# Optimization experiments

Hardware: AMD Instinct MI355X
Metric: run time of the kernel (lower is better)

The kernel has to match this reference:

```python
import jax, jax.numpy as jnp
import numpy as np

B, CIN, H, W = 256, 1280, 7, 7
A, NCLS, HID, NGT = 9, 20, 128, 40
OUT_DIM = 5 * A + NCLS  # 65


def setup_inputs() -> dict:
    key = jax.random.key(0)
    ks = jax.random.split(key, 8)
    features = jax.random.normal(ks[0], (B, CIN, H, W), jnp.float32)
    # grid: (x, y) centers of each feature cell, in feature-map coordinates
    grid = jax.random.uniform(ks[1], (B, H, W, 2), jnp.float32) * 7.0
    # GT boxes (x1, y1, x2, y2, class), padded count NGT per image
    xy1 = jax.random.uniform(ks[2], (B, NGT, 2), jnp.float32) * 5.0
    wh = jax.random.uniform(ks[3], (B, NGT, 2), jnp.float32) * 2.0 + 0.5
    cls = jax.random.randint(ks[4], (B, NGT, 1), 0, NCLS).astype(jnp.float32)
    bboxes = jnp.concatenate([xy1, xy1 + wh, cls], axis=-1)
    # anchor shapes (w, h) as in SingleStageDetector.__init__
    anc = jnp.array([[1.0, 1], [2, 2], [3, 3], [4, 4], [5, 5],
                     [2, 3], [3, 2], [3, 5], [5, 3]], jnp.float32)
    W1 = jax.random.normal(ks[5], (HID, CIN), jnp.float32) * 0.02
    b1 = jnp.zeros((HID,), jnp.float32)
    W2 = jax.random.normal(ks[6], (OUT_DIM, HID), jnp.float32) * 0.02
    b2 = jnp.zeros((OUT_DIM,), jnp.float32)
    return dict(features=features, grid=grid, bboxes=bboxes, anc=anc,
                W1=W1, b1=b1, W2=W2, b2=b2)


def reference(features, grid, bboxes, anc, W1, b1, W2, b2):
    Bx = features.shape[0]
    # --- PredictionNetwork (inference mode; dropout is identity at eval) ---
    h = jnp.einsum('bchw,oc->bohw', features, W1) + b1[None, :, None, None]
    h = jax.nn.leaky_relu(h, negative_slope=0.01)
    out = jnp.einsum('bchw,oc->bohw', h, W2) + b2[None, :, None, None]
    conf_scores = jax.nn.sigmoid(out[:, 4 * A:5 * A])          # (B, A, H, W)
    offsets = out[:, :4 * A].reshape(Bx, A, 4, H, W)
    offsets = jnp.concatenate(
        [jax.nn.sigmoid(offsets[:, :, :2]) - 0.5, offsets[:, :, 2:]], axis=2)
    class_scores = out[:, 5 * A:]                               # (B, C, H, W)
    # --- GenerateAnchor: (B, A, H, W, 4) as (x_tl, y_tl, x_br, y_br) ---
    ctr = grid[:, None]                    # (B, 1, H, W, 2)
    half = anc[None, :, None, None, :] / 2  # (1, A, 1, 1, 2)
    anchors = jnp.concatenate([ctr - half, ctr + half], axis=-1)
    # --- IoU: (B, A*H*W, N) ---
    P = anchors.reshape(Bx, -1, 4)          # (B, AHW, 4)
    gt = bboxes[..., :4]                    # (B, N, 4)
    tl = jnp.maximum(P[:, :, None, :2], gt[:, None, :, :2])
    br = jnp.minimum(P[:, :, None, 2:], gt[:, None, :, 2:])
    inter = jnp.prod(jnp.clip(br - tl, 0.0), axis=-1)  # (B, AHW, N)
    # torch code zeroes intersections for proposals with any coord <= 0
    legal = (jnp.min(P, axis=-1) > 0)[..., None]
    inter = inter * legal
    p_area = ((P[:, :, 2] - P[:, :, 0]) * (P[:, :, 3] - P[:, :, 1]))[:, :, None]
    g_area = ((gt[:, :, 2] - gt[:, :, 0]) * (gt[:, :, 3] - gt[:, :, 1]))[:, None, :]
    iou_mat = inter / (g_area + p_area - inter)
    return (conf_scores, offsets, class_scores, iou_mat)
```

## Files before the change

### kernel.cpp

```cpp
#include <hip/hip_runtime.h>


#define CIN_  1280
#define HW_   49
#define HID_  128
#define OUTD_ 65
#define NGT_  40
#define NP_   441
#define NCH   20

#define CONF_OFF 0
#define OFFS_OFF 112896
#define CLS_OFF  564480
#define IOU_OFF  815360

#define W1F_U32  81920

#define SF_STRIDE 644
#define SF_SIZE   (49 * SF_STRIDE)

typedef __bf16 bf16x8 __attribute__((ext_vector_type(8)));
typedef float  f32x4  __attribute__((ext_vector_type(4)));

__device__ __forceinline__ unsigned pack2bf(float lo, float hi) {
    unsigned a = __float_as_uint(lo);
    unsigned b = __float_as_uint(hi);
    a = (a + 0x7FFFu + ((a >> 16) & 1u)) >> 16;
    b = (b + 0x7FFFu + ((b >> 16) & 1u)) >> 16;
    return a | (b << 16);
}
__device__ __forceinline__ float bflo(unsigned u) { return __uint_as_float(u << 16); }
__device__ __forceinline__ float bfhi(unsigned u) { return __uint_as_float(u & 0xFFFF0000u); }
__device__ __forceinline__ float sigmoidf_(float v) { return 1.f / (1.f + __expf(-v)); }

__device__ __forceinline__ bf16x8 ld_frag(const unsigned* p) {
    union { uint4 u; bf16x8 v; } x;
    x.u = *(const uint4*)p;
    return x.v;
}
__device__ __forceinline__ bf16x8 as_bf(uint4 u) {
    union { uint4 u; bf16x8 v; } x; x.u = u; return x.v;
}

__global__ __launch_bounds__(256) void prep_w1(const float* __restrict__ W1,
                                               unsigned* __restrict__ gW1f) {
    int X = blockIdx.x * 256 + threadIdx.x;
    int sub  = X & 3;
    int lane = (X >> 2) & 63;
    int r    = X >> 8;
    int ks   = r & 1;
    int w    = (r >> 1) & 7;
    int ch   = r >> 4;
    int o = w * 16 + (lane & 15);
    int c = ch * 64 + ks * 32 + (lane >> 4) * 8 + sub * 2;
    float2 f = *(const float2*)(W1 + o * CIN_ + c);
    gW1f[X] = pack2bf(f.x, f.y);
}

__global__ __launch_bounds__(512) void fused_kernel(
    const float* __restrict__ F,
    const float* __restrict__ grid,
    const float* __restrict__ bbox,
    const float* __restrict__ anc,
    const unsigned* __restrict__ gW1f,
    const float* __restrict__ B1,
    const float* __restrict__ W2,
    const float* __restrict__ B2,
    float* __restrict__ out)
{
    __shared__ unsigned lds[SF_SIZE];
    unsigned* smF = lds;
    unsigned* smH = lds;
    float* smP = (float*)(lds + 3136);
    float* smG = (float*)(lds + 3136 + 2646);

    const int tid  = threadIdx.x;
    const int b    = blockIdx.x;
    const int lane = tid & 63;
    const int w    = tid >> 6;
    const int quad = lane >> 4;
    const int m16  = lane & 15;

    const float* Fb = F + b * (CIN_ * HW_);

    for (int i = tid; i < 640 * 49; i += 512) {
        int cp = i / 49;
        int hw = i - cp * 49;
        const float* s = Fb + (2 * cp) * HW_ + hw;
        smF[hw * SF_STRIDE + cp] = pack2bf(s[0], s[HW_]);
    }
    __syncthreads();

    const int row3 = (m16 == 0) ? 48 : (m16 - 1);
    const unsigned* Bb[4] = {
        smF + (0 * 16 + m16) * SF_STRIDE + quad * 4,
        smF + (1 * 16 + m16) * SF_STRIDE + quad * 4,
        smF + (2 * 16 + m16) * SF_STRIDE + quad * 4,
        smF + row3 * SF_STRIDE + quad * 4
    };

    const uint4* Aw = (const uint4*)gW1f + (w * 2) * 64 + lane;

    f32x4 acc[4];
    #pragma unroll
    for (int nt = 0; nt < 4; ++nt) acc[nt] = (f32x4)(0.f);

    uint4 a0 = Aw[0];
    uint4 a1 = Aw[64];
    for (int ch = 0; ch < NCH; ++ch) {
        uint4 na0, na1;
        if (ch < NCH - 1) {
            na0 = Aw[(ch + 1) * 1024];
            na1 = Aw[(ch + 1) * 1024 + 64];
        }
        const int coff = ch * 32;
        bf16x8 aa0 = as_bf(a0);
        bf16x8 aa1 = as_bf(a1);
        #pragma unroll
        for (int nt = 0; nt < 4; ++nt) {
            bf16x8 b0 = ld_frag(Bb[nt] + coff);
            bf16x8 b1 = ld_frag(Bb[nt] + coff + 16);
            acc[nt] = __builtin_amdgcn_mfma_f32_16x16x32_bf16(aa0, b0, acc[nt], 0, 0, 0);
            acc[nt] = __builtin_amdgcn_mfma_f32_16x16x32_bf16(aa1, b1, acc[nt], 0, 0, 0);
        }
        a0 = na0; a1 = na1;
    }

    __syncthreads();

    #pragma unroll
    for (int nt = 0; nt < 4; ++nt) {
        int hw = (nt < 3) ? (nt * 16 + m16) : ((m16 == 0) ? 48 : -1);
        if (hw >= 0) {
            #pragma unroll
            for (int rp = 0; rp < 2; ++rp) {
                int o0 = w * 16 + quad * 4 + 2 * rp;
                float v0 = acc[nt][2 * rp]     + B1[o0];
                float v1 = acc[nt][2 * rp + 1] + B1[o0 + 1];
                v0 = v0 > 0.f ? v0 : 0.01f * v0;
                v1 = v1 > 0.f ? v1 : 0.01f * v1;
                smH[(o0 >> 1) * HW_ + hw] = pack2bf(v0, v1);
            }
        }
    }

    if (tid < NP_) {
        int pp = tid, a = pp / 49, r = pp - a * 49;
        float cx = grid[b * 98 + 2 * r], cy = grid[b * 98 + 2 * r + 1];
        float hx = anc[2 * a] * 0.5f,    hy = anc[2 * a + 1] * 0.5f;
        float x1 = cx - hx, y1 = cy - hy, x2 = cx + hx, y2 = cy + hy;
        smP[pp * 6 + 0] = x1; smP[pp * 6 + 1] = y1;
        smP[pp * 6 + 2] = x2; smP[pp * 6 + 3] = y2;
        smP[pp * 6 + 4] = (x2 - x1) * (y2 - y1);
        smP[pp * 6 + 5] = (fminf(fminf(x1, y1), fminf(x2, y2)) > 0.f) ? 1.f : 0.f;
    }
    if (tid >= 472) {
        int g = tid - 472;
        float x1 = bbox[b * 200 + g * 5 + 0];
        float y1 = bbox[b * 200 + g * 5 + 1];
        float x2 = bbox[b * 200 + g * 5 + 2];
        float y2 = bbox[b * 200 + g * 5 + 3];
        smG[g * 5 + 0] = x1; smG[g * 5 + 1] = y1;
        smG[g * 5 + 2] = x2; smG[g * 5 + 3] = y2;
        smG[g * 5 + 4] = (x2 - x1) * (y2 - y1);
    }
    __syncthreads();

    for (int idx = tid; idx < OUTD_ * HW_; idx += 512) {
        int o2 = idx / 49;
        int hw = idx - o2 * 49;
        const float2* wr = (const float2*)(W2 + o2 * HID_);
        float s0 = 0.f, s1 = 0.f;
        #pragma unroll 8
        for (int k2 = 0; k2 < 64; ++k2) {
            unsigned hp = smH[k2 * HW_ + hw];
            float2 wv = wr[k2];
            s0 = fmaf(wv.x, bflo(hp), s0);
            s1 = fmaf(wv.y, bfhi(hp), s1);
        }
        float a = B2[o2] + (s0 + s1);

        unsigned int dst;
        float val;
        if (o2 < 36) {
            int an = o2 >> 2, kk = o2 & 3;
            val = (kk < 2) ? (sigmoidf_(a) - 0.5f) : a;
            dst = OFFS_OFF + b * 1764 + an * 196 + kk * 49 + hw;
        } else if (o2 < 45) {
            val = sigmoidf_(a);
            dst = CONF_OFF + b * 441 + (o2 - 36) * 49 + hw;
        } else {
            val = a;
            dst = CLS_OFF + b * 980 + (o2 - 45) * 49 + hw;
        }
        out[dst] = val;
    }

    for (int idx = tid; idx < NP_ * NGT_; idx += 512) {
        int pp = idx / 40;
        int g  = idx - pp * 40;
        const float* P = smP + pp * 6;
        const float* G = smG + g * 5;
        float tlx = fmaxf(P[0], G[0]);
        float tly = fmaxf(P[1], G[1]);
        float brx = fminf(P[2], G[2]);
        float bry = fminf(P[3], G[3]);
        float dx = fmaxf(brx - tlx, 0.f);
        float dy = fmaxf(bry - tly, 0.f);
        float inter = dx * dy * P[5];
        out[IOU_OFF + b * (NP_ * NGT_) + idx] = inter / (G[4] + P[4] - inter);
    }
}

__global__ __launch_bounds__(512) void fused_fallback(
    const float* __restrict__ F, const float* __restrict__ grid,
    const float* __restrict__ bbox, const float* __restrict__ anc,
    const float* __restrict__ W1, const float* __restrict__ B1,
    const float* __restrict__ W2, const float* __restrict__ B2,
    float* __restrict__ out)
{
    __shared__ unsigned lds[4608 + 2304 + 6272];
    unsigned* smA = lds;
    unsigned* smB = lds + 4608;
    float*    smH = (float*)(lds + 4608 + 2304);
    float* smP = (float*)lds;
    float* smG = (float*)(lds + 4608);

    const int tid  = threadIdx.x;
    const int b    = blockIdx.x;
    const int lane = tid & 63;
    const int w    = tid >> 6;
    const int quad = lane >> 4;
    const int m16  = lane & 15;
    const float* Fb = F + b * (CIN_ * HW_);

    f32x4 acc[4];
    #pragma unroll
    for (int nt = 0; nt < 4; ++nt) acc[nt] = (f32x4)(0.f);

    for (int ch = 0; ch < NCH; ++ch) {
        const int c0 = ch * 64;
        __syncthreads();
        #pragma unroll
        for (int rr = 0; rr < 8; ++rr) {
            int pi = tid + rr * 512;
            int o = pi >> 5, cp = pi & 31;
            float2 fx = *(const float2*)(W1 + o * CIN_ + c0 + 2 * cp);
            smA[o * 36 + cp] = pack2bf(fx.x, fx.y);
        }
        for (int pi = tid; pi < 32 * 49; pi += 512) {
            int cp = pi / 49;
            int hw = pi - cp * 49;
            const float* src = Fb + (c0 + 2 * cp) * HW_ + hw;
            smB[hw * 36 + cp] = pack2bf(src[0], src[HW_]);
        }
        __syncthreads();
        const unsigned* Ab = smA + (w * 16 + m16) * 36 + quad * 4;
        const unsigned* Bb = smB + m16 * 36 + quad * 4;
        #pragma unroll
        for (int ks = 0; ks < 2; ++ks) {
            bf16x8 af = ld_frag(Ab + ks * 16);
            #pragma unroll
            for (int nt = 0; nt < 4; ++nt) {
                bf16x8 bf = ld_frag(Bb + nt * 16 * 36 + ks * 16);
                acc[nt] = __builtin_amdgcn_mfma_f32_16x16x32_bf16(af, bf, acc[nt], 0, 0, 0);
            }
        }
    }
    #pragma unroll
    for (int nt = 0; nt < 4; ++nt) {
        int hw = nt * 16 + m16;
        if (hw < HW_) {
            #pragma unroll
            for (int r = 0; r < 4; ++r) {
                int o = w * 16 + quad * 4 + r;
                float v = acc[nt][r] + B1[o];
                v = v > 0.f ? v : 0.01f * v;
                smH[o * HW_ + hw] = v;
            }
        }
    }
    __syncthreads();
    if (tid < NP_) {
        int pp = tid, a = pp / 49, r = pp - a * 49;
        float cx = grid[b * 98 + 2 * r], cy = grid[b * 98 + 2 * r + 1];
        float hx = anc[2 * a] * 0.5f,    hy = anc[2 * a + 1] * 0.5f;
        float x1 = cx - hx, y1 = cy - hy, x2 = cx + hx, y2 = cy + hy;
        smP[pp * 6 + 0] = x1; smP[pp * 6 + 1] = y1;
        smP[pp * 6 + 2] = x2; smP[pp * 6 + 3] = y2;
        smP[pp * 6 + 4] = (x2 - x1) * (y2 - y1);
        smP[pp * 6 + 5] = (fminf(fminf(x1, y1), fminf(x2, y2)) > 0.f) ? 1.f : 0.f;
    }
    if (tid >= 472) {
        int g = tid - 472;
        float x1 = bbox[b * 200 + g * 5 + 0];
        float y1 = bbox[b * 200 + g * 5 + 1];
        float x2 = bbox[b * 200 + g * 5 + 2];
        float y2 = bbox[b * 200 + g * 5 + 3];
        smG[g * 5 + 0] = x1; smG[g * 5 + 1] = y1;
        smG[g * 5 + 2] = x2; smG[g * 5 + 3] = y2;
        smG[g * 5 + 4] = (x2 - x1) * (y2 - y1);
    }
    for (int idx = tid; idx < OUTD_ * HW_; idx += 512) {
        int o2 = idx / 49;
        int hw = idx - o2 * 49;
        const float4* wr = (const float4*)(W2 + o2 * HID_);
        const float*  hc = smH + hw;
        float s0 = 0.f, s1 = 0.f, s2 = 0.f, s3 = 0.f;
        #pragma unroll 8
        for (int k4 = 0; k4 < 32; ++k4) {
            float4 wv = wr[k4];
            s0 = fmaf(wv.x, hc[(4 * k4 + 0) * HW_], s0);
            s1 = fmaf(wv.y, hc[(4 * k4 + 1) * HW_], s1);
            s2 = fmaf(wv.z, hc[(4 * k4 + 2) * HW_], s2);
            s3 = fmaf(wv.w, hc[(4 * k4 + 3) * HW_], s3);
        }
        float a = B2[o2] + ((s0 + s1) + (s2 + s3));
        unsigned int dst; float val;
        if (o2 < 36) { int an = o2 >> 2, kk = o2 & 3;
            val = (kk < 2) ? (sigmoidf_(a) - 0.5f) : a;
            dst = OFFS_OFF + b * 1764 + an * 196 + kk * 49 + hw;
        } else if (o2 < 45) { val = sigmoidf_(a);
            dst = CONF_OFF + b * 441 + (o2 - 36) * 49 + hw;
        } else { val = a;
            dst = CLS_OFF + b * 980 + (o2 - 45) * 49 + hw; }
        out[dst] = val;
    }
    __syncthreads();
    for (int idx = tid; idx < NP_ * NGT_; idx += 512) {
        int pp = idx / 40;
        int g  = idx - pp * 40;
        const float* P = smP + pp * 6;
        const float* G = smG + g * 5;
        float tlx = fmaxf(P[0], G[0]);
        float tly = fmaxf(P[1], G[1]);
        float brx = fminf(P[2], G[2]);
        float bry = fminf(P[3], G[3]);
        float dx = fmaxf(brx - tlx, 0.f);
        float dy = fmaxf(bry - tly, 0.f);
        float inter = dx * dy * P[5];
        out[IOU_OFF + b * (NP_ * NGT_) + idx] = inter / (G[4] + P[4] - inter);
    }
}

extern "C" void kernel_launch(void* const* d_in, const int* in_sizes, int n_in,
                              void* d_out, int out_size, void* d_ws, size_t ws_size,
                              hipStream_t stream) {
    const float* F  = (const float*)d_in[0];
    const float* G  = (const float*)d_in[1];
    const float* BB = (const float*)d_in[2];
    const float* AN = (const float*)d_in[3];
    const float* W1 = (const float*)d_in[4];
    const float* B1 = (const float*)d_in[5];
    const float* W2 = (const float*)d_in[6];
    const float* B2 = (const float*)d_in[7];
    float* out = (float*)d_out;

    if (ws_size >= (size_t)W1F_U32 * 4) {
        unsigned* gW1f = (unsigned*)d_ws;
        prep_w1<<<320, 256, 0, stream>>>(W1, gW1f);
        fused_kernel<<<256, 512, 0, stream>>>(F, G, BB, AN, gW1f, B1, W2, B2, out);
    } else {
        fused_fallback<<<256, 512, 0, stream>>>(F, G, BB, AN, W1, B1, W2, B2, out);
    }
}
```

Before: 141.3 us.

## Split GEMM1 along K across four blocks per image, add MFMA GEMM2 epilogue kernel

The first GEMM is split along the input-channel dimension into four blocks per image (1024 blocks instead of 256), so more CUs work on the feature load and MFMA loop. Each block writes bf16 partial sums to workspace, and the IoU work is spread across the four blocks. A second kernel reduces the partials, applies bias and leaky-ReLU, and runs the 65x128 head through MFMA with pre-packed bf16 W2. In exchange it adds extra launches, a workspace round-trip for the partials, and more rounding because the partials are stored in bf16.

```diff
diff --git a/kernel.cpp b/kernel.cpp
--- a/kernel.cpp
+++ b/kernel.cpp
@@ -7,17 +7,17 @@
 #define OUTD_ 65
 #define NGT_  40
 #define NP_   441
-#define NCH   20
 
 #define CONF_OFF 0
 #define OFFS_OFF 112896
 #define CLS_OFF  564480
 #define IOU_OFF  815360
 
-#define W1F_U32  81920
-
-#define SF_STRIDE 644
-#define SF_SIZE   (49 * SF_STRIDE)
+#define WS_W1F   0
+#define WS_W2F   81920
+#define WS_PART  87040
+#define WS_NEED_FULL ((87040u + 3211264u) * 4u)
+#define WS_NEED_MID  (81920u * 4u)
 
 typedef __bf16 bf16x8 __attribute__((ext_vector_type(8)));
 typedef float  f32x4  __attribute__((ext_vector_type(4)));
@@ -42,37 +42,161 @@
     union { uint4 u; bf16x8 v; } x; x.u = u; return x.v;
 }
 
-__global__ __launch_bounds__(256) void prep_w1(const float* __restrict__ W1,
-                                               unsigned* __restrict__ gW1f) {
+__global__ __launch_bounds__(256) void prep_w1f(const float* __restrict__ W1,
+                                                unsigned* __restrict__ g) {
     int X = blockIdx.x * 256 + threadIdx.x;
-    int sub  = X & 3;
-    int lane = (X >> 2) & 63;
-    int r    = X >> 8;
-    int ks   = r & 1;
-    int w    = (r >> 1) & 7;
-    int ch   = r >> 4;
-    int o = w * 16 + (lane & 15);
-    int c = ch * 64 + ks * 32 + (lane >> 4) * 8 + sub * 2;
-    float2 f = *(const float2*)(W1 + o * CIN_ + c);
-    gW1f[X] = pack2bf(f.x, f.y);
-}
-
-__global__ __launch_bounds__(512) void fused_kernel(
-    const float* __restrict__ F,
-    const float* __restrict__ grid,
-    const float* __restrict__ bbox,
-    const float* __restrict__ anc,
+    int sub = X & 3, lane = (X >> 2) & 63, f = X >> 8;
+    int mt = f & 7, K32 = f >> 3;
+    int o = mt * 16 + (lane & 15);
+    int c = K32 * 32 + (lane >> 4) * 8 + sub * 2;
+    float2 v = *(const float2*)(W1 + o * CIN_ + c);
+    g[X] = pack2bf(v.x, v.y);
+}
+
+__global__ __launch_bounds__(256) void prep_w2f(const float* __restrict__ W2,
+                                                unsigned* __restrict__ g) {
+    int X = blockIdx.x * 256 + threadIdx.x;
+    int sub = X & 3, lane = (X >> 2) & 63, f = X >> 8;
+    int mt2 = f % 5, ks2 = f / 5;
+    int o2 = mt2 * 16 + (lane & 15);
+    int c = ks2 * 32 + (lane >> 4) * 8 + sub * 2;
+    unsigned val = 0;
+    if (o2 < OUTD_) {
+        float2 v = *(const float2*)(W2 + o2 * HID_ + c);
+        val = pack2bf(v.x, v.y);
+    }
+    g[X] = val;
+}
+
+__global__ __launch_bounds__(256) void gemm1_partial(
+    const float* __restrict__ F, const float* __restrict__ grid,
+    const float* __restrict__ bbox, const float* __restrict__ anc,
     const unsigned* __restrict__ gW1f,
-    const float* __restrict__ B1,
-    const float* __restrict__ W2,
-    const float* __restrict__ B2,
+    unsigned* __restrict__ wsp, float* __restrict__ out)
+{
+    __shared__ __align__(16) unsigned smF[49 * 164];
+    float* smP = (float*)smF;
+    float* smG = (float*)smF + 2646;
+
+    const int tid  = threadIdx.x;
+    const int b    = blockIdx.x >> 2;
+    const int ksp  = blockIdx.x & 3;
+    const int lane = tid & 63;
+    const int w    = tid >> 6;
+    const int quad = lane >> 4;
+    const int m16  = lane & 15;
+
+    const float* Fb = F + b * (CIN_ * HW_) + ksp * 320 * HW_;
+
+    for (int idx = tid; idx < 1960; idx += 256) {
+        int cb = idx / 49;
+        int hw = idx - cb * 49;
+        const float* s = Fb + cb * 392 + hw;
+        float v0 = s[0],   v1 = s[49],  v2 = s[98],  v3 = s[147];
+        float v4 = s[196], v5 = s[245], v6 = s[294], v7 = s[343];
+        uint4 pk;
+        pk.x = pack2bf(v0, v1); pk.y = pack2bf(v2, v3);
+        pk.z = pack2bf(v4, v5); pk.w = pack2bf(v6, v7);
+        *(uint4*)(smF + hw * 164 + cb * 4) = pk;
+    }
+    __syncthreads();
+
+    const int row3 = (m16 == 0) ? 48 : (m16 - 1);
+    const unsigned* Bb[4] = {
+        smF + m16 * 164 + quad * 4,
+        smF + (16 + m16) * 164 + quad * 4,
+        smF + (32 + m16) * 164 + quad * 4,
+        smF + row3 * 164 + quad * 4
+    };
+
+    const int mt0 = w * 2, mt1 = mt0 + 1;
+    const int K32b = ksp * 10;
+    const uint4* Ap0 = (const uint4*)gW1f + (K32b * 8 + mt0) * 64 + lane;
+    const uint4* Ap1 = (const uint4*)gW1f + (K32b * 8 + mt1) * 64 + lane;
+
+    f32x4 acc0[4], acc1[4];
+    #pragma unroll
+    for (int nt = 0; nt < 4; ++nt) { acc0[nt] = (f32x4)(0.f); acc1[nt] = (f32x4)(0.f); }
+
+    uint4 a0 = Ap0[0], a1 = Ap1[0];
+    for (int k = 0; k < 10; ++k) {
+        uint4 n0, n1;
+        if (k < 9) { n0 = Ap0[(k + 1) * 512]; n1 = Ap1[(k + 1) * 512]; }
+        bf16x8 A0 = as_bf(a0), A1 = as_bf(a1);
+        const int co = k * 16;
+        #pragma unroll
+        for (int nt = 0; nt < 4; ++nt) {
+            bf16x8 Bf = ld_frag(Bb[nt] + co);
+            acc0[nt] = __builtin_amdgcn_mfma_f32_16x16x32_bf16(A0, Bf, acc0[nt], 0, 0, 0);
+            acc1[nt] = __builtin_amdgcn_mfma_f32_16x16x32_bf16(A1, Bf, acc1[nt], 0, 0, 0);
+        }
+        a0 = n0; a1 = n1;
+    }
+
+    const unsigned pbase = (unsigned)(b * 4 + ksp) * 64u;
+    #pragma unroll
+    for (int m = 0; m < 2; ++m) {
+        const f32x4* ac = m ? acc1 : acc0;
+        int mtg = w * 2 + m;
+        #pragma unroll
+        for (int nt = 0; nt < 4; ++nt) {
+            int hw = (nt < 3) ? (nt * 16 + m16) : ((m16 == 0) ? 48 : -1);
+            if (hw >= 0) {
+                #pragma unroll
+                for (int rp = 0; rp < 2; ++rp) {
+                    int op = mtg * 8 + quad * 2 + rp;
+                    wsp[(pbase + op) * 49u + hw] = pack2bf(ac[nt][2 * rp], ac[nt][2 * rp + 1]);
+                }
+            }
+        }
+    }
+    __syncthreads();
+
+    for (int pp = tid; pp < NP_; pp += 256) {
+        int a = pp / 49, r = pp - a * 49;
+        float cx = grid[b * 98 + 2 * r], cy = grid[b * 98 + 2 * r + 1];
+        float hx = anc[2 * a] * 0.5f,    hy = anc[2 * a + 1] * 0.5f;
+        float x1 = cx - hx, y1 = cy - hy, x2 = cx + hx, y2 = cy + hy;
+        smP[pp * 6 + 0] = x1; smP[pp * 6 + 1] = y1;
+        smP[pp * 6 + 2] = x2; smP[pp * 6 + 3] = y2;
+        smP[pp * 6 + 4] = (x2 - x1) * (y2 - y1);
+        smP[pp * 6 + 5] = (fminf(fminf(x1, y1), fminf(x2, y2)) > 0.f) ? 1.f : 0.f;
+    }
+    if (tid < NGT_) {
+        int g = tid;
+        float x1 = bbox[b * 200 + g * 5 + 0];
+        float y1 = bbox[b * 200 + g * 5 + 1];
+        float x2 = bbox[b * 200 + g * 5 + 2];
+        float y2 = bbox[b * 200 + g * 5 + 3];
+        smG[g * 5 + 0] = x1; smG[g * 5 + 1] = y1;
+        smG[g * 5 + 2] = x2; smG[g * 5 + 3] = y2;
+        smG[g * 5 + 4] = (x2 - x1) * (y2 - y1);
+    }
+    __syncthreads();
+
+    for (int ii = tid; ii < 4410; ii += 256) {
+        int idx = ksp * 4410 + ii;
+        int p = idx / 40;
+        int g = idx - p * 40;
+        const float* P = smP + p * 6;
+        const float* G = smG + g * 5;
+        float tlx = fmaxf(P[0], G[0]);
+        float tly = fmaxf(P[1], G[1]);
+        float brx = fminf(P[2], G[2]);
+        float bry = fminf(P[3], G[3]);
+        float dx = fmaxf(brx - tlx, 0.f);
+        float dy = fmaxf(bry - tly, 0.f);
+        float inter = dx * dy * P[5];
+        out[IOU_OFF + b * (NP_ * NGT_) + idx] = inter / (G[4] + P[4] - inter);
+    }
+}
+
+__global__ __launch_bounds__(320) void gemm2_epilogue(
+    const unsigned* __restrict__ wsp, const unsigned* __restrict__ gW2f,
+    const float* __restrict__ B1, const float* __restrict__ B2,
     float* __restrict__ out)
 {
-    __shared__ unsigned lds[SF_SIZE];
-    unsigned* smF = lds;
-    unsigned* smH = lds;
-    float* smP = (float*)(lds + 3136);
-    float* smG = (float*)(lds + 3136 + 2646);
+    __shared__ __align__(16) unsigned smHT[49 * 68];
 
     const int tid  = threadIdx.x;
     const int b    = blockIdx.x;
@@ -81,6 +205,91 @@
     const int quad = lane >> 4;
     const int m16  = lane & 15;
 
+    const uint4* Aw2 = (const uint4*)gW2f + w * 64 + lane;
+    uint4 af0 = Aw2[0], af1 = Aw2[320], af2 = Aw2[640], af3 = Aw2[960];
+
+    const unsigned* pb = wsp + b * 12544;
+    for (int j = tid; j < 3136; j += 320) {
+        int op = j / 49;
+        int hw = j - op * 49;
+        const unsigned* p = pb + op * 49 + hw;
+        unsigned u0 = p[0], u1 = p[3136], u2 = p[6272], u3 = p[9408];
+        float v0 = ((bflo(u0) + bflo(u1)) + (bflo(u2) + bflo(u3))) + B1[2 * op];
+        float v1 = ((bfhi(u0) + bfhi(u1)) + (bfhi(u2) + bfhi(u3))) + B1[2 * op + 1];
+        v0 = v0 > 0.f ? v0 : 0.01f * v0;
+        v1 = v1 > 0.f ? v1 : 0.01f * v1;
+        smHT[hw * 68 + op] = pack2bf(v0, v1);
+    }
+    __syncthreads();
+
+    const int row3 = (m16 == 0) ? 48 : (m16 - 1);
+    const unsigned* Bb[4] = {
+        smHT + m16 * 68 + quad * 4,
+        smHT + (16 + m16) * 68 + quad * 4,
+        smHT + (32 + m16) * 68 + quad * 4,
+        smHT + row3 * 68 + quad * 4
+    };
+    f32x4 acc[4];
+    #pragma unroll
+    for (int nt = 0; nt < 4; ++nt) acc[nt] = (f32x4)(0.f);
+    uint4 afs[4] = { af0, af1, af2, af3 };
+    #pragma unroll
+    for (int ks2 = 0; ks2 < 4; ++ks2) {
+        bf16x8 A = as_bf(afs[ks2]);
+        const int co = ks2 * 16;
+        #pragma unroll
+        for (int nt = 0; nt < 4; ++nt) {
+            bf16x8 Bf = ld_frag(Bb[nt] + co);
+            acc[nt] = __builtin_amdgcn_mfma_f32_16x16x32_bf16(A, Bf, acc[nt], 0, 0, 0);
+        }
+    }
+
+    #pragma unroll
+    for (int nt = 0; nt < 4; ++nt) {
+        int hw = (nt < 3) ? (nt * 16 + m16) : ((m16 == 0) ? 48 : -1);
+        if (hw < 0) continue;
+        #pragma unroll
+        for (int r = 0; r < 4; ++r) {
+            int o2 = w * 16 + quad * 4 + r;
+            if (o2 >= OUTD_) continue;
+            float a = acc[nt][r] + B2[o2];
+            unsigned dst; float val;
+            if (o2 < 36) {
+                int an = o2 >> 2, kk = o2 & 3;
+                val = (kk < 2) ? (sigmoidf_(a) - 0.5f) : a;
+                dst = OFFS_OFF + b * 1764 + an * 196 + kk * 49 + hw;
+            } else if (o2 < 45) {
+                val = sigmoidf_(a);
+                dst = CONF_OFF + b * 441 + (o2 - 36) * 49 + hw;
+            } else {
+                val = a;
+                dst = CLS_OFF + b * 980 + (o2 - 45) * 49 + hw;
+            }
+            out[dst] = val;
+        }
+    }
+}
+
+#define SF_STRIDE 644
+__global__ __launch_bounds__(512) void fused_single(
+    const float* __restrict__ F, const float* __restrict__ grid,
+    const float* __restrict__ bbox, const float* __restrict__ anc,
+    const unsigned* __restrict__ gW1f, const float* __restrict__ B1,
+    const float* __restrict__ W2, const float* __restrict__ B2,
+    float* __restrict__ out)
+{
+    __shared__ __align__(16) unsigned lds[49 * SF_STRIDE];
+    unsigned* smF = lds;
+    unsigned* smH = lds;
+    float* smP = (float*)(lds + 3136);
+    float* smG = (float*)(lds + 3136 + 2646);
+
+    const int tid  = threadIdx.x;
+    const int b    = blockIdx.x;
+    const int lane = tid & 63;
+    const int w    = tid >> 6;
+    const int quad = lane >> 4;
+    const int m16  = lane & 15;
     const float* Fb = F + b * (CIN_ * HW_);
 
     for (int i = tid; i < 640 * 49; i += 512) {
@@ -93,39 +302,32 @@
 
     const int row3 = (m16 == 0) ? 48 : (m16 - 1);
     const unsigned* Bb[4] = {
-        smF + (0 * 16 + m16) * SF_STRIDE + quad * 4,
-        smF + (1 * 16 + m16) * SF_STRIDE + quad * 4,
-        smF + (2 * 16 + m16) * SF_STRIDE + quad * 4,
+        smF + m16 * SF_STRIDE + quad * 4,
+        smF + (16 + m16) * SF_STRIDE + quad * 4,
+        smF + (32 + m16) * SF_STRIDE + quad * 4,
         smF + row3 * SF_STRIDE + quad * 4
     };
-
-    const uint4* Aw = (const uint4*)gW1f + (w * 2) * 64 + lane;
+    const uint4* Aw = (const uint4*)gW1f + w * 64 + lane;
 
     f32x4 acc[4];
     #pragma unroll
     for (int nt = 0; nt < 4; ++nt) acc[nt] = (f32x4)(0.f);
 
-    uint4 a0 = Aw[0];
-    uint4 a1 = Aw[64];
-    for (int ch = 0; ch < NCH; ++ch) {
-        uint4 na0, na1;
-        if (ch < NCH - 1) {
-            na0 = Aw[(ch + 1) * 1024];
-            na1 = Aw[(ch + 1) * 1024 + 64];
-        }
+    uint4 a0 = Aw[0], a1 = Aw[512];
+    for (int ch = 0; ch < 20; ++ch) {
+        uint4 n0, n1;
+        if (ch < 19) { n0 = Aw[(ch + 1) * 1024]; n1 = Aw[(ch + 1) * 1024 + 512]; }
         const int coff = ch * 32;
-        bf16x8 aa0 = as_bf(a0);
-        bf16x8 aa1 = as_bf(a1);
+        bf16x8 A0 = as_bf(a0), A1 = as_bf(a1);
         #pragma unroll
         for (int nt = 0; nt < 4; ++nt) {
             bf16x8 b0 = ld_frag(Bb[nt] + coff);
             bf16x8 b1 = ld_frag(Bb[nt] + coff + 16);
-            acc[nt] = __builtin_amdgcn_mfma_f32_16x16x32_bf16(aa0, b0, acc[nt], 0, 0, 0);
-            acc[nt] = __builtin_amdgcn_mfma_f32_16x16x32_bf16(aa1, b1, acc[nt], 0, 0, 0);
-        }
-        a0 = na0; a1 = na1;
-    }
-
+            acc[nt] = __builtin_amdgcn_mfma_f32_16x16x32_bf16(A0, b0, acc[nt], 0, 0, 0);
+            acc[nt] = __builtin_amdgcn_mfma_f32_16x16x32_bf16(A1, b1, acc[nt], 0, 0, 0);
+        }
+        a0 = n0; a1 = n1;
+    }
     __syncthreads();
 
     #pragma unroll
@@ -143,7 +345,6 @@
             }
         }
     }
-
     if (tid < NP_) {
         int pp = tid, a = pp / 49, r = pp - a * 49;
         float cx = grid[b * 98 + 2 * r], cy = grid[b * 98 + 2 * r + 1];
@@ -179,9 +380,7 @@
             s1 = fmaf(wv.y, bfhi(hp), s1);
         }
         float a = B2[o2] + (s0 + s1);
-
-        unsigned int dst;
-        float val;
+        unsigned dst; float val;
         if (o2 < 36) {
             int an = o2 >> 2, kk = o2 & 3;
             val = (kk < 2) ? (sigmoidf_(a) - 0.5f) : a;
@@ -195,7 +394,6 @@
         }
         out[dst] = val;
     }
-
     for (int idx = tid; idx < NP_ * NGT_; idx += 512) {
         int pp = idx / 40;
         int g  = idx - pp * 40;
@@ -219,7 +417,7 @@
     const float* __restrict__ W2, const float* __restrict__ B2,
     float* __restrict__ out)
 {
-    __shared__ unsigned lds[4608 + 2304 + 6272];
+    __shared__ __align__(16) unsigned lds[4608 + 2304 + 6272];
     unsigned* smA = lds;
     unsigned* smB = lds + 4608;
     float*    smH = (float*)(lds + 4608 + 2304);
@@ -238,7 +436,7 @@
     #pragma unroll
     for (int nt = 0; nt < 4; ++nt) acc[nt] = (f32x4)(0.f);
 
-    for (int ch = 0; ch < NCH; ++ch) {
+    for (int ch = 0; ch < 20; ++ch) {
         const int c0 = ch * 64;
         __syncthreads();
         #pragma unroll
@@ -316,7 +514,7 @@
             s3 = fmaf(wv.w, hc[(4 * k4 + 3) * HW_], s3);
         }
         float a = B2[o2] + ((s0 + s1) + (s2 + s3));
-        unsigned int dst; float val;
+        unsigned dst; float val;
         if (o2 < 36) { int an = o2 >> 2, kk = o2 & 3;
             val = (kk < 2) ? (sigmoidf_(a) - 0.5f) : a;
             dst = OFFS_OFF + b * 1764 + an * 196 + kk * 49 + hw;
@@ -355,11 +553,19 @@
     const float* W2 = (const float*)d_in[6];
     const float* B2 = (const float*)d_in[7];
     float* out = (float*)d_out;
-
-    if (ws_size >= (size_t)W1F_U32 * 4) {
-        unsigned* gW1f = (unsigned*)d_ws;
-        prep_w1<<<320, 256, 0, stream>>>(W1, gW1f);
-        fused_kernel<<<256, 512, 0, stream>>>(F, G, BB, AN, gW1f, B1, W2, B2, out);
+    unsigned* wsu = (unsigned*)d_ws;
+
+    if (ws_size >= (size_t)WS_NEED_FULL) {
+        prep_w1f<<<320, 256, 0, stream>>>(W1, wsu + WS_W1F);
+        prep_w2f<<<20, 256, 0, stream>>>(W2, wsu + WS_W2F);
+        gemm1_partial<<<1024, 256, 0, stream>>>(F, G, BB, AN, wsu + WS_W1F,
+                                                wsu + WS_PART, out);
+        gemm2_epilogue<<<256, 320, 0, stream>>>(wsu + WS_PART, wsu + WS_W2F,
+                                                B1, B2, out);
+    } else if (ws_size >= (size_t)WS_NEED_MID) {
+        prep_w1f<<<320, 256, 0, stream>>>(W1, wsu + WS_W1F);
+        fused_single<<<256, 512, 0, stream>>>(F, G, BB, AN, wsu + WS_W1F,
+                                              B1, W2, B2, out);
     } else {
         fused_fallback<<<256, 512, 0, stream>>>(F, G, BB, AN, W1, B1, W2, B2, out);
     }
```

New measurement: 140.5 us. About the same (-0.6%).
